# Kernel tuning notes

Hardware: AMD Instinct MI355X
Metric: run time of the kernel (lower is better)

## Reference

```python
import jax, jax.numpy as jnp
import numpy as np

WINDOW = 7
HEADS = 8


def setup_inputs() -> dict:
    key = jax.random.key(0)
    ks = jax.random.split(key, 6)
    B, L, C = 4096, WINDOW * WINDOW, 256
    x = jax.random.normal(ks[0], (B, L, C), dtype=jnp.float32)
    relative_index = jax.random.randint(ks[1], (L * L,), 0, (2 * WINDOW - 1) ** 2, dtype=jnp.int32)
    qkv_w = jax.random.normal(ks[2], (C, 3 * C), dtype=jnp.float32) * 0.02
    qkv_b = jnp.zeros((3 * C,), dtype=jnp.float32)
    rel_bias = jax.random.normal(ks[3], ((2 * WINDOW - 1) ** 2, HEADS), dtype=jnp.float32) * 0.02
    proj_w = jax.random.normal(ks[4], (C, C), dtype=jnp.float32) * 0.02
    proj_b = jnp.zeros((C,), dtype=jnp.float32)
    return {"x": x, "relative_index": relative_index, "qkv_w": qkv_w, "qkv_b": qkv_b,
            "rel_bias": rel_bias, "proj_w": proj_w, "proj_b": proj_b}


def reference(x, relative_index, qkv_w, qkv_b, rel_bias, proj_w, proj_b):
    B, L, C = x.shape
    H = HEADS
    D = C // H
    scale = D ** -0.5
    # qkv projection -> [3, B, H, L, D]
    qkv = (x @ qkv_w + qkv_b).reshape(B, L, 3, H, D).transpose(2, 0, 3, 1, 4)
    q, k, v = qkv[0], qkv[1], qkv[2]
    attn = jnp.einsum('bhld,bhmd->bhlm', q * scale, k)  # [B,H,L,L]
    # gather relative position bias: [L*L, H] -> [H, L, L]
    bias = rel_bias[relative_index].reshape(L, L, H).transpose(2, 0, 1)
    attn = jax.nn.softmax(attn + bias[None], axis=-1)
    out = jnp.einsum('bhlm,bhmd->blhd', attn, v).reshape(B, L, C)
    return out @ proj_w + proj_b
```

## Files before the change

### kernel.cpp

```cpp
#include <hip/hip_runtime.h>


typedef short s8v __attribute__((ext_vector_type(8)));
typedef short s4v __attribute__((ext_vector_type(4)));
typedef float f4  __attribute__((ext_vector_type(4)));

#define MFMA(a,b,c) __builtin_amdgcn_mfma_f32_16x16x32_bf16((a),(b),(c),0,0,0)

__device__ __forceinline__ unsigned short f2bf(float f) {
    unsigned u = __float_as_uint(f);
    u = u + 0x7fffu + ((u >> 16) & 1u);
    return (unsigned short)(u >> 16);
}

__device__ __forceinline__ unsigned pkbf(float lo, float hi) {
    unsigned r;
    asm("v_cvt_pk_bf16_f32 %0, %1, %2" : "=v"(r) : "v"(lo), "v"(hi));
    return r;
}

__global__ void prep(const float* __restrict__ qkv_w, const float* __restrict__ proj_w,
                     const float* __restrict__ rel_bias, const int* __restrict__ rel_idx,
                     unsigned short* __restrict__ wq, unsigned short* __restrict__ wp,
                     float* __restrict__ biasT2)
{
    int idx = blockIdx.x * blockDim.x + threadIdx.x;
    int stride = gridDim.x * blockDim.x;
    for (int i = idx; i < 48*8*64*8; i += stride) {
        int j = i & 7, l = (i >> 3) & 63, ks = (i >> 9) & 7, nt = i >> 12;
        int k = ks*32 + (l >> 4)*8 + j;
        int n = nt*16 + (l & 15);
        wq[i] = f2bf(qkv_w[k*768 + n]);
    }
    for (int i = idx; i < 16*8*64*8; i += stride) {
        int j = i & 7, l = (i >> 3) & 63, ks = (i >> 9) & 7, nt = i >> 12;
        int k = ks*32 + (l >> 4)*8 + j;
        int n = nt*16 + (l & 15);
        wp[i] = f2bf(proj_w[k*256 + n]);
    }
    for (int i = idx; i < 8*64*64; i += stride) {
        int k = i & 63, q = (i >> 6) & 63, h = i >> 12;
        float v;
        if (k < 49) v = (q < 49) ? rel_bias[rel_idx[q*49 + k]*8 + h] : 0.f;
        else        v = -1e30f;
        biasT2[i] = v;
    }
}

__global__ __launch_bounds__(512, 2) void kall(
    const float* __restrict__ x, const float* __restrict__ qkv_b,
    const unsigned short* __restrict__ wq, const float* __restrict__ biasT2,
    const unsigned short* __restrict__ wp, const float* __restrict__ proj_b,
    float* __restrict__ out)
{
    __shared__ __align__(16) unsigned short xs[4][8][64][8];
    __shared__ __align__(16) unsigned short osd[64][264];

    const int b    = blockIdx.x;
    const int tid  = threadIdx.x;
    const int w    = tid >> 6;
    const int lane = tid & 63;
    const int ln   = lane & 15;
    const int g    = lane >> 4;

    const float* xb = x + (size_t)b * (49*256);
    for (int i = tid; i < 4096; i += 512) {
        int r = i >> 6, c4 = i & 63;
        float4 v = make_float4(0.f, 0.f, 0.f, 0.f);
        if (r < 49) v = ((const float4*)xb)[r*64 + c4];
        uint2 o;
        o.x = pkbf(v.x, v.y);
        o.y = pkbf(v.z, v.w);
        int mt = r >> 4, lnr = r & 15;
        int c  = c4 * 4;
        int ks = c >> 5, gg = (c >> 3) & 3, j0 = c & 7;
        *(uint2*)&xs[mt][ks][(gg*16 + lnr) ^ ks][j0] = o;
    }
    __syncthreads();

    const float scale = 0.17677669529663687f;
    const int h = w;

    f4 qa[2][4], ka[2][4], va[4][2];
    #pragma unroll
    for (int dh = 0; dh < 2; ++dh)
        #pragma unroll
        for (int mt = 0; mt < 4; ++mt) {
            qa[dh][mt] = (f4){0.f,0.f,0.f,0.f};
            ka[dh][mt] = (f4){0.f,0.f,0.f,0.f};
            va[mt][dh] = (f4){0.f,0.f,0.f,0.f};
        }

    #pragma unroll
    for (int ks = 0; ks < 8; ++ks) {
        s8v xf[4];
        #pragma unroll
        for (int mt = 0; mt < 4; ++mt)
            xf[mt] = *(const s8v*)&xs[mt][ks][lane ^ ks][0];
        s8v wfq[2], wfk[2], wfv[2];
        #pragma unroll
        for (int dh = 0; dh < 2; ++dh) {
            wfq[dh] = *(const s8v*)&wq[(size_t)((( 2*h+dh)*8 + ks)*64 + lane) * 8];
            wfk[dh] = *(const s8v*)&wq[(size_t)(((16+2*h+dh)*8 + ks)*64 + lane) * 8];
            wfv[dh] = *(const s8v*)&wq[(size_t)(((32+2*h+dh)*8 + ks)*64 + lane) * 8];
        }
        #pragma unroll
        for (int dh = 0; dh < 2; ++dh)
            #pragma unroll
            for (int mt = 0; mt < 4; ++mt) {
                qa[dh][mt] = MFMA(wfq[dh], xf[mt], qa[dh][mt]);
                ka[dh][mt] = MFMA(wfk[dh], xf[mt], ka[dh][mt]);
                va[mt][dh] = MFMA(xf[mt], wfv[dh], va[mt][dh]);
            }
    }

    float4 bq[2], bk[2]; float bv[2];
    #pragma unroll
    for (int dh = 0; dh < 2; ++dh) {
        bq[dh] = *(const float4*)&qkv_b[       h*32 + dh*16 + g*4];
        bk[dh] = *(const float4*)&qkv_b[256 +  h*32 + dh*16 + g*4];
        bv[dh] = qkv_b[512 + h*32 + dh*16 + ln];
    }

    s8v qf[4], kf[4], vf[2][2];
    #pragma unroll
    for (int t = 0; t < 4; ++t) {
        union { s8v s; unsigned u[4]; } qu, ku;
        qu.u[0] = pkbf((qa[0][t][0] + bq[0].x)*scale, (qa[0][t][1] + bq[0].y)*scale);
        qu.u[1] = pkbf((qa[0][t][2] + bq[0].z)*scale, (qa[0][t][3] + bq[0].w)*scale);
        qu.u[2] = pkbf((qa[1][t][0] + bq[1].x)*scale, (qa[1][t][1] + bq[1].y)*scale);
        qu.u[3] = pkbf((qa[1][t][2] + bq[1].z)*scale, (qa[1][t][3] + bq[1].w)*scale);
        ku.u[0] = pkbf( ka[0][t][0] + bk[0].x,  ka[0][t][1] + bk[0].y);
        ku.u[1] = pkbf( ka[0][t][2] + bk[0].z,  ka[0][t][3] + bk[0].w);
        ku.u[2] = pkbf( ka[1][t][0] + bk[1].x,  ka[1][t][1] + bk[1].y);
        ku.u[3] = pkbf( ka[1][t][2] + bk[1].z,  ka[1][t][3] + bk[1].w);
        qf[t] = qu.s;
        kf[t] = ku.s;
    }
    #pragma unroll
    for (int ksp = 0; ksp < 2; ++ksp)
        #pragma unroll
        for (int dh = 0; dh < 2; ++dh) {
            union { s8v s; unsigned u[4]; } vu;
            vu.u[0] = pkbf(va[2*ksp  ][dh][0] + bv[dh], va[2*ksp  ][dh][1] + bv[dh]);
            vu.u[1] = pkbf(va[2*ksp  ][dh][2] + bv[dh], va[2*ksp  ][dh][3] + bv[dh]);
            vu.u[2] = pkbf(va[2*ksp+1][dh][0] + bv[dh], va[2*ksp+1][dh][1] + bv[dh]);
            vu.u[3] = pkbf(va[2*ksp+1][dh][2] + bv[dh], va[2*ksp+1][dh][3] + bv[dh]);
            vf[ksp][dh] = vu.s;
        }

    #pragma unroll
    for (int qt = 0; qt < 4; ++qt) {
        f4 bias4[4];
        #pragma unroll
        for (int kt = 0; kt < 4; ++kt)
            bias4[kt] = *(const f4*)&biasT2[(size_t)(h*64 + qt*16 + ln)*64 + kt*16 + g*4];

        __builtin_amdgcn_s_setprio(1);
        f4 st[4];
        #pragma unroll
        for (int kt = 0; kt < 4; ++kt) {
            f4 z = (f4){0.f,0.f,0.f,0.f};
            st[kt] = MFMA(kf[kt], qf[qt], z);
        }
        __builtin_amdgcn_s_setprio(0);

        float pr[16];
        float sum = 0.f;
        #pragma unroll
        for (int kt = 0; kt < 4; ++kt)
            #pragma unroll
            for (int r = 0; r < 4; ++r) {
                float e = __expf(st[kt][r] + bias4[kt][r]);
                pr[kt*4 + r] = e;
                sum += e;
            }
        sum += __shfl_xor(sum, 16);
        sum += __shfl_xor(sum, 32);
        float rinv = 1.f / sum;

        s8v pa[2];
        #pragma unroll
        for (int ksp = 0; ksp < 2; ++ksp) {
            union { s8v s; unsigned u[4]; } pu;
            #pragma unroll
            for (int i2 = 0; i2 < 4; ++i2)
                pu.u[i2] = pkbf(pr[8*ksp + 2*i2] * rinv, pr[8*ksp + 2*i2 + 1] * rinv);
            pa[ksp] = pu.s;
        }

        __builtin_amdgcn_s_setprio(1);
        f4 oacc[2];
        oacc[0] = (f4){0.f,0.f,0.f,0.f};
        oacc[1] = (f4){0.f,0.f,0.f,0.f};
        #pragma unroll
        for (int ksp = 0; ksp < 2; ++ksp)
            #pragma unroll
            for (int dh = 0; dh < 2; ++dh)
                oacc[dh] = MFMA(pa[ksp], vf[ksp][dh], oacc[dh]);
        __builtin_amdgcn_s_setprio(0);

        #pragma unroll
        for (int dh = 0; dh < 2; ++dh)
            #pragma unroll
            for (int r = 0; r < 4; ++r)
                osd[qt*16 + g*4 + r][h*32 + dh*16 + ln] = f2bf(oacc[dh][r]);
    }
    __syncthreads();

    f4 acc[4][2];
    #pragma unroll
    for (int mt = 0; mt < 4; ++mt)
        #pragma unroll
        for (int t = 0; t < 2; ++t)
            acc[mt][t] = (f4){0.f,0.f,0.f,0.f};

    #pragma unroll
    for (int ks = 0; ks < 8; ++ks) {
        s8v av[4], bw[2];
        #pragma unroll
        for (int mt = 0; mt < 4; ++mt)
            av[mt] = *(const s8v*)&osd[mt*16 + ln][ks*32 + g*8];
        #pragma unroll
        for (int t = 0; t < 2; ++t) {
            int nt = w*2 + t;
            bw[t] = *(const s8v*)&wp[(size_t)((nt*8 + ks)*64 + lane) * 8];
        }
        #pragma unroll
        for (int mt = 0; mt < 4; ++mt)
            #pragma unroll
            for (int t = 0; t < 2; ++t)
                acc[mt][t] = MFMA(av[mt], bw[t], acc[mt][t]);
    }

    float* ob = out + (size_t)b * (49*256);
    #pragma unroll
    for (int t = 0; t < 2; ++t) {
        int n = (w*2 + t)*16 + ln;
        float pb = proj_b[n];
        #pragma unroll
        for (int mt = 0; mt < 4; ++mt)
            #pragma unroll
            for (int r = 0; r < 4; ++r) {
                int q = mt*16 + g*4 + r;
                if (q < 49)
                    ob[q*256 + n] = acc[mt][t][r] + pb;
            }
    }
}

extern "C" void kernel_launch(void* const* d_in, const int* in_sizes, int n_in,
                              void* d_out, int out_size, void* d_ws, size_t ws_size,
                              hipStream_t stream)
{
    (void)n_in; (void)out_size; (void)ws_size;
    const float* x        = (const float*)d_in[0];
    const int*   rel_idx  = (const int*)  d_in[1];
    const float* qkv_w    = (const float*)d_in[2];
    const float* qkv_b    = (const float*)d_in[3];
    const float* rel_bias = (const float*)d_in[4];
    const float* proj_w   = (const float*)d_in[5];
    const float* proj_b   = (const float*)d_in[6];
    float* out = (float*)d_out;

    const int B = in_sizes[0] / (49*256);

    unsigned short* wq = (unsigned short*)d_ws;
    unsigned short* wp = wq + 48*8*64*8;
    float* biasT2 = (float*)((char*)d_ws + 524288);

    prep<<<256, 256, 0, stream>>>(qkv_w, proj_w, rel_bias, rel_idx, wq, wp, biasT2);
    kall<<<B, 512, 0, stream>>>(x, qkv_b, wq, biasT2, wp, proj_b, out);
}
```

Measured before the change: 274.0 us.

## Process eight windows per block with double-buffered register prefetch of x

Each block now loops over 8 windows instead of one. The next window's x is loaded into registers during the QKV MFMA phase and written into a second LDS buffer before attention, so global load latency overlaps with compute. This amortizes block launch and bias setup, but the grid shrinks to 512 blocks. That leaves fewer blocks than CUs times occupancy, and register pressure rises from the 8 float4 prefetch registers.

```diff
diff --git a/kernel.cpp b/kernel.cpp
--- a/kernel.cpp
+++ b/kernel.cpp
@@ -2,7 +2,6 @@
 
 
 typedef short s8v __attribute__((ext_vector_type(8)));
-typedef short s4v __attribute__((ext_vector_type(4)));
 typedef float f4  __attribute__((ext_vector_type(4)));
 
 #define MFMA(a,b,c) __builtin_amdgcn_mfma_f32_16x16x32_bf16((a),(b),(c),0,0,0)
@@ -17,6 +16,34 @@
     unsigned r;
     asm("v_cvt_pk_bf16_f32 %0, %1, %2" : "=v"(r) : "v"(lo), "v"(hi));
     return r;
+}
+
+__device__ __forceinline__ void load_pf(const float* __restrict__ xb,
+                                        float4 pf[8], int tid) {
+    #pragma unroll
+    for (int ii = 0; ii < 8; ++ii) {
+        int i = tid + ii*512;
+        float4 v = make_float4(0.f, 0.f, 0.f, 0.f);
+        if ((i >> 6) < 49) v = ((const float4*)xb)[i];
+        pf[ii] = v;
+    }
+}
+
+__device__ __forceinline__ void cvt_write_xs(const float4 pf[8],
+                                             unsigned short (*xsb)[8][64][8],
+                                             int tid) {
+    #pragma unroll
+    for (int ii = 0; ii < 8; ++ii) {
+        int i = tid + ii*512;
+        int r = i >> 6, c4 = i & 63;
+        uint2 o;
+        o.x = pkbf(pf[ii].x, pf[ii].y);
+        o.y = pkbf(pf[ii].z, pf[ii].w);
+        int mt = r >> 4, lnr = r & 15;
+        int c  = c4 * 4;
+        int ks = c >> 5, gg = (c >> 3) & 3, j0 = c & 7;
+        *(uint2*)&xsb[mt][ks][(gg*16 + lnr) ^ ks][j0] = o;
+    }
 }
 
 __global__ void prep(const float* __restrict__ qkv_w, const float* __restrict__ proj_w,
@@ -51,68 +78,23 @@
     const float* __restrict__ x, const float* __restrict__ qkv_b,
     const unsigned short* __restrict__ wq, const float* __restrict__ biasT2,
     const unsigned short* __restrict__ wp, const float* __restrict__ proj_b,
-    float* __restrict__ out)
+    float* __restrict__ out, int B)
 {
-    __shared__ __align__(16) unsigned short xs[4][8][64][8];
+    __shared__ __align__(16) unsigned short xs2[2][4][8][64][8];
     __shared__ __align__(16) unsigned short osd[64][264];
 
-    const int b    = blockIdx.x;
     const int tid  = threadIdx.x;
     const int w    = tid >> 6;
     const int lane = tid & 63;
     const int ln   = lane & 15;
     const int g    = lane >> 4;
 
-    const float* xb = x + (size_t)b * (49*256);
-    for (int i = tid; i < 4096; i += 512) {
-        int r = i >> 6, c4 = i & 63;
-        float4 v = make_float4(0.f, 0.f, 0.f, 0.f);
-        if (r < 49) v = ((const float4*)xb)[r*64 + c4];
-        uint2 o;
-        o.x = pkbf(v.x, v.y);
-        o.y = pkbf(v.z, v.w);
-        int mt = r >> 4, lnr = r & 15;
-        int c  = c4 * 4;
-        int ks = c >> 5, gg = (c >> 3) & 3, j0 = c & 7;
-        *(uint2*)&xs[mt][ks][(gg*16 + lnr) ^ ks][j0] = o;
-    }
-    __syncthreads();
+    const int W    = 8;
+    const int win0 = blockIdx.x * W;
+    const int nw   = (B - win0 < W) ? (B - win0) : W;
 
     const float scale = 0.17677669529663687f;
     const int h = w;
-
-    f4 qa[2][4], ka[2][4], va[4][2];
-    #pragma unroll
-    for (int dh = 0; dh < 2; ++dh)
-        #pragma unroll
-        for (int mt = 0; mt < 4; ++mt) {
-            qa[dh][mt] = (f4){0.f,0.f,0.f,0.f};
-            ka[dh][mt] = (f4){0.f,0.f,0.f,0.f};
-            va[mt][dh] = (f4){0.f,0.f,0.f,0.f};
-        }
-
-    #pragma unroll
-    for (int ks = 0; ks < 8; ++ks) {
-        s8v xf[4];
-        #pragma unroll
-        for (int mt = 0; mt < 4; ++mt)
-            xf[mt] = *(const s8v*)&xs[mt][ks][lane ^ ks][0];
-        s8v wfq[2], wfk[2], wfv[2];
-        #pragma unroll
-        for (int dh = 0; dh < 2; ++dh) {
-            wfq[dh] = *(const s8v*)&wq[(size_t)((( 2*h+dh)*8 + ks)*64 + lane) * 8];
-            wfk[dh] = *(const s8v*)&wq[(size_t)(((16+2*h+dh)*8 + ks)*64 + lane) * 8];
-            wfv[dh] = *(const s8v*)&wq[(size_t)(((32+2*h+dh)*8 + ks)*64 + lane) * 8];
-        }
-        #pragma unroll
-        for (int dh = 0; dh < 2; ++dh)
-            #pragma unroll
-            for (int mt = 0; mt < 4; ++mt) {
-                qa[dh][mt] = MFMA(wfq[dh], xf[mt], qa[dh][mt]);
-                ka[dh][mt] = MFMA(wfk[dh], xf[mt], ka[dh][mt]);
-                va[mt][dh] = MFMA(xf[mt], wfv[dh], va[mt][dh]);
-            }
-    }
 
     float4 bq[2], bk[2]; float bv[2];
     #pragma unroll
@@ -122,130 +104,179 @@
         bv[dh] = qkv_b[512 + h*32 + dh*16 + ln];
     }
 
-    s8v qf[4], kf[4], vf[2][2];
-    #pragma unroll
-    for (int t = 0; t < 4; ++t) {
-        union { s8v s; unsigned u[4]; } qu, ku;
-        qu.u[0] = pkbf((qa[0][t][0] + bq[0].x)*scale, (qa[0][t][1] + bq[0].y)*scale);
-        qu.u[1] = pkbf((qa[0][t][2] + bq[0].z)*scale, (qa[0][t][3] + bq[0].w)*scale);
-        qu.u[2] = pkbf((qa[1][t][0] + bq[1].x)*scale, (qa[1][t][1] + bq[1].y)*scale);
-        qu.u[3] = pkbf((qa[1][t][2] + bq[1].z)*scale, (qa[1][t][3] + bq[1].w)*scale);
-        ku.u[0] = pkbf( ka[0][t][0] + bk[0].x,  ka[0][t][1] + bk[0].y);
-        ku.u[1] = pkbf( ka[0][t][2] + bk[0].z,  ka[0][t][3] + bk[0].w);
-        ku.u[2] = pkbf( ka[1][t][0] + bk[1].x,  ka[1][t][1] + bk[1].y);
-        ku.u[3] = pkbf( ka[1][t][2] + bk[1].z,  ka[1][t][3] + bk[1].w);
-        qf[t] = qu.s;
-        kf[t] = ku.s;
-    }
-    #pragma unroll
-    for (int ksp = 0; ksp < 2; ++ksp)
-        #pragma unroll
-        for (int dh = 0; dh < 2; ++dh) {
-            union { s8v s; unsigned u[4]; } vu;
-            vu.u[0] = pkbf(va[2*ksp  ][dh][0] + bv[dh], va[2*ksp  ][dh][1] + bv[dh]);
-            vu.u[1] = pkbf(va[2*ksp  ][dh][2] + bv[dh], va[2*ksp  ][dh][3] + bv[dh]);
-            vu.u[2] = pkbf(va[2*ksp+1][dh][0] + bv[dh], va[2*ksp+1][dh][1] + bv[dh]);
-            vu.u[3] = pkbf(va[2*ksp+1][dh][2] + bv[dh], va[2*ksp+1][dh][3] + bv[dh]);
-            vf[ksp][dh] = vu.s;
-        }
-
-    #pragma unroll
-    for (int qt = 0; qt < 4; ++qt) {
-        f4 bias4[4];
-        #pragma unroll
-        for (int kt = 0; kt < 4; ++kt)
-            bias4[kt] = *(const f4*)&biasT2[(size_t)(h*64 + qt*16 + ln)*64 + kt*16 + g*4];
-
-        __builtin_amdgcn_s_setprio(1);
-        f4 st[4];
-        #pragma unroll
-        for (int kt = 0; kt < 4; ++kt) {
-            f4 z = (f4){0.f,0.f,0.f,0.f};
-            st[kt] = MFMA(kf[kt], qf[qt], z);
-        }
-        __builtin_amdgcn_s_setprio(0);
-
-        float pr[16];
-        float sum = 0.f;
-        #pragma unroll
-        for (int kt = 0; kt < 4; ++kt)
-            #pragma unroll
-            for (int r = 0; r < 4; ++r) {
-                float e = __expf(st[kt][r] + bias4[kt][r]);
-                pr[kt*4 + r] = e;
-                sum += e;
-            }
-        sum += __shfl_xor(sum, 16);
-        sum += __shfl_xor(sum, 32);
-        float rinv = 1.f / sum;
-
-        s8v pa[2];
-        #pragma unroll
-        for (int ksp = 0; ksp < 2; ++ksp) {
-            union { s8v s; unsigned u[4]; } pu;
-            #pragma unroll
-            for (int i2 = 0; i2 < 4; ++i2)
-                pu.u[i2] = pkbf(pr[8*ksp + 2*i2] * rinv, pr[8*ksp + 2*i2 + 1] * rinv);
-            pa[ksp] = pu.s;
-        }
-
-        __builtin_amdgcn_s_setprio(1);
-        f4 oacc[2];
-        oacc[0] = (f4){0.f,0.f,0.f,0.f};
-        oacc[1] = (f4){0.f,0.f,0.f,0.f};
+    float4 pf[8];
+    load_pf(x + (size_t)win0 * (49*256), pf, tid);
+    cvt_write_xs(pf, xs2[0], tid);
+    __syncthreads();
+
+    for (int iw = 0; iw < nw; ++iw) {
+        const int b = win0 + iw;
+        unsigned short (*xsb)[8][64][8] = xs2[iw & 1];
+        const bool hn = (iw + 1 < nw);
+
+        if (hn) load_pf(x + (size_t)(b+1) * (49*256), pf, tid);
+
+        f4 qa[2][4], ka[2][4], va[4][2];
+        #pragma unroll
+        for (int dh = 0; dh < 2; ++dh)
+            #pragma unroll
+            for (int mt = 0; mt < 4; ++mt) {
+                qa[dh][mt] = (f4){0.f,0.f,0.f,0.f};
+                ka[dh][mt] = (f4){0.f,0.f,0.f,0.f};
+                va[mt][dh] = (f4){0.f,0.f,0.f,0.f};
+            }
+
+        #pragma unroll
+        for (int ks = 0; ks < 8; ++ks) {
+            s8v xf[4];
+            #pragma unroll
+            for (int mt = 0; mt < 4; ++mt)
+                xf[mt] = *(const s8v*)&xsb[mt][ks][lane ^ ks][0];
+            s8v wfq[2], wfk[2], wfv[2];
+            #pragma unroll
+            for (int dh = 0; dh < 2; ++dh) {
+                wfq[dh] = *(const s8v*)&wq[(size_t)((( 2*h+dh)*8 + ks)*64 + lane) * 8];
+                wfk[dh] = *(const s8v*)&wq[(size_t)(((16+2*h+dh)*8 + ks)*64 + lane) * 8];
+                wfv[dh] = *(const s8v*)&wq[(size_t)(((32+2*h+dh)*8 + ks)*64 + lane) * 8];
+            }
+            #pragma unroll
+            for (int dh = 0; dh < 2; ++dh)
+                #pragma unroll
+                for (int mt = 0; mt < 4; ++mt) {
+                    qa[dh][mt] = MFMA(wfq[dh], xf[mt], qa[dh][mt]);
+                    ka[dh][mt] = MFMA(wfk[dh], xf[mt], ka[dh][mt]);
+                    va[mt][dh] = MFMA(xf[mt], wfv[dh], va[mt][dh]);
+                }
+        }
+
+        s8v qf[4], kf[4], vf[2][2];
+        #pragma unroll
+        for (int t = 0; t < 4; ++t) {
+            union { s8v s; unsigned u[4]; } qu, ku;
+            qu.u[0] = pkbf((qa[0][t][0] + bq[0].x)*scale, (qa[0][t][1] + bq[0].y)*scale);
+            qu.u[1] = pkbf((qa[0][t][2] + bq[0].z)*scale, (qa[0][t][3] + bq[0].w)*scale);
+            qu.u[2] = pkbf((qa[1][t][0] + bq[1].x)*scale, (qa[1][t][1] + bq[1].y)*scale);
+            qu.u[3] = pkbf((qa[1][t][2] + bq[1].z)*scale, (qa[1][t][3] + bq[1].w)*scale);
+            ku.u[0] = pkbf( ka[0][t][0] + bk[0].x,  ka[0][t][1] + bk[0].y);
+            ku.u[1] = pkbf( ka[0][t][2] + bk[0].z,  ka[0][t][3] + bk[0].w);
+            ku.u[2] = pkbf( ka[1][t][0] + bk[1].x,  ka[1][t][1] + bk[1].y);
+            ku.u[3] = pkbf( ka[1][t][2] + bk[1].z,  ka[1][t][3] + bk[1].w);
+            qf[t] = qu.s;
+            kf[t] = ku.s;
+        }
         #pragma unroll
         for (int ksp = 0; ksp < 2; ++ksp)
             #pragma unroll
+            for (int dh = 0; dh < 2; ++dh) {
+                union { s8v s; unsigned u[4]; } vu;
+                vu.u[0] = pkbf(va[2*ksp  ][dh][0] + bv[dh], va[2*ksp  ][dh][1] + bv[dh]);
+                vu.u[1] = pkbf(va[2*ksp  ][dh][2] + bv[dh], va[2*ksp  ][dh][3] + bv[dh]);
+                vu.u[2] = pkbf(va[2*ksp+1][dh][0] + bv[dh], va[2*ksp+1][dh][1] + bv[dh]);
+                vu.u[3] = pkbf(va[2*ksp+1][dh][2] + bv[dh], va[2*ksp+1][dh][3] + bv[dh]);
+                vf[ksp][dh] = vu.s;
+            }
+
+        if (hn) cvt_write_xs(pf, xs2[(iw + 1) & 1], tid);
+
+        #pragma unroll
+        for (int qt = 0; qt < 4; ++qt) {
+            f4 bias4[4];
+            #pragma unroll
+            for (int kt = 0; kt < 4; ++kt)
+                bias4[kt] = *(const f4*)&biasT2[(size_t)(h*64 + qt*16 + ln)*64 + kt*16 + g*4];
+
+            __builtin_amdgcn_s_setprio(1);
+            f4 st[4];
+            #pragma unroll
+            for (int kt = 0; kt < 4; ++kt) {
+                f4 z = (f4){0.f,0.f,0.f,0.f};
+                st[kt] = MFMA(kf[kt], qf[qt], z);
+            }
+            __builtin_amdgcn_s_setprio(0);
+
+            float pr[16];
+            float sum = 0.f;
+            #pragma unroll
+            for (int kt = 0; kt < 4; ++kt)
+                #pragma unroll
+                for (int r = 0; r < 4; ++r) {
+                    float e = __expf(st[kt][r] + bias4[kt][r]);
+                    pr[kt*4 + r] = e;
+                    sum += e;
+                }
+            sum += __shfl_xor(sum, 16);
+            sum += __shfl_xor(sum, 32);
+            float rinv = 1.f / sum;
+
+            s8v pa[2];
+            #pragma unroll
+            for (int ksp = 0; ksp < 2; ++ksp) {
+                union { s8v s; unsigned u[4]; } pu;
+                #pragma unroll
+                for (int i2 = 0; i2 < 4; ++i2)
+                    pu.u[i2] = pkbf(pr[8*ksp + 2*i2] * rinv, pr[8*ksp + 2*i2 + 1] * rinv);
+                pa[ksp] = pu.s;
+            }
+
+            __builtin_amdgcn_s_setprio(1);
+            f4 oacc[2];
+            oacc[0] = (f4){0.f,0.f,0.f,0.f};
+            oacc[1] = (f4){0.f,0.f,0.f,0.f};
+            #pragma unroll
+            for (int ksp = 0; ksp < 2; ++ksp)
+                #pragma unroll
+                for (int dh = 0; dh < 2; ++dh)
+                    oacc[dh] = MFMA(pa[ksp], vf[ksp][dh], oacc[dh]);
+            __builtin_amdgcn_s_setprio(0);
+
+            #pragma unroll
             for (int dh = 0; dh < 2; ++dh)
-                oacc[dh] = MFMA(pa[ksp], vf[ksp][dh], oacc[dh]);
-        __builtin_amdgcn_s_setprio(0);
-
-        #pragma unroll
-        for (int dh = 0; dh < 2; ++dh)
-            #pragma unroll
-            for (int r = 0; r < 4; ++r)
-                osd[qt*16 + g*4 + r][h*32 + dh*16 + ln] = f2bf(oacc[dh][r]);
-    }
-    __syncthreads();
-
-    f4 acc[4][2];
-    #pragma unroll
-    for (int mt = 0; mt < 4; ++mt)
-        #pragma unroll
-        for (int t = 0; t < 2; ++t)
-            acc[mt][t] = (f4){0.f,0.f,0.f,0.f};
-
-    #pragma unroll
-    for (int ks = 0; ks < 8; ++ks) {
-        s8v av[4], bw[2];
+                #pragma unroll
+                for (int r = 0; r < 4; ++r)
+                    osd[qt*16 + g*4 + r][h*32 + dh*16 + ln] = f2bf(oacc[dh][r]);
+        }
+        __syncthreads();
+
+        f4 acc[4][2];
         #pragma unroll
         for (int mt = 0; mt < 4; ++mt)
-            av[mt] = *(const s8v*)&osd[mt*16 + ln][ks*32 + g*8];
+            #pragma unroll
+            for (int t = 0; t < 2; ++t)
+                acc[mt][t] = (f4){0.f,0.f,0.f,0.f};
+
+        #pragma unroll
+        for (int ks = 0; ks < 8; ++ks) {
+            s8v av[4], bw[2];
+            #pragma unroll
+            for (int mt = 0; mt < 4; ++mt)
+                av[mt] = *(const s8v*)&osd[mt*16 + ln][ks*32 + g*8];
+            #pragma unroll
+            for (int t = 0; t < 2; ++t) {
+                int nt = w*2 + t;
+                bw[t] = *(const s8v*)&wp[(size_t)((nt*8 + ks)*64 + lane) * 8];
+            }
+            #pragma unroll
+            for (int mt = 0; mt < 4; ++mt)
+                #pragma unroll
+                for (int t = 0; t < 2; ++t)
+                    acc[mt][t] = MFMA(av[mt], bw[t], acc[mt][t]);
+        }
+
+        float* ob = out + (size_t)b * (49*256);
         #pragma unroll
         for (int t = 0; t < 2; ++t) {
-            int nt = w*2 + t;
-            bw[t] = *(const s8v*)&wp[(size_t)((nt*8 + ks)*64 + lane) * 8];
-        }
-        #pragma unroll
-        for (int mt = 0; mt < 4; ++mt)
-            #pragma unroll
-            for (int t = 0; t < 2; ++t)
-                acc[mt][t] = MFMA(av[mt], bw[t], acc[mt][t]);
-    }
-
-    float* ob = out + (size_t)b * (49*256);
-    #pragma unroll
-    for (int t = 0; t < 2; ++t) {
-        int n = (w*2 + t)*16 + ln;
-        float pb = proj_b[n];
-        #pragma unroll
-        for (int mt = 0; mt < 4; ++mt)
-            #pragma unroll
-            for (int r = 0; r < 4; ++r) {
-                int q = mt*16 + g*4 + r;
-                if (q < 49)
-                    ob[q*256 + n] = acc[mt][t][r] + pb;
-            }
+            int n = (w*2 + t)*16 + ln;
+            float pb = proj_b[n];
+            #pragma unroll
+            for (int mt = 0; mt < 4; ++mt)
+                #pragma unroll
+                for (int r = 0; r < 4; ++r) {
+                    int q = mt*16 + g*4 + r;
+                    if (q < 49)
+                        ob[q*256 + n] = acc[mt][t][r] + pb;
+                }
+        }
+        __syncthreads();
     }
 }
 
@@ -264,11 +295,13 @@
     float* out = (float*)d_out;
 
     const int B = in_sizes[0] / (49*256);
+    const int W = 8;
+    const int nb = (B + W - 1) / W;
 
     unsigned short* wq = (unsigned short*)d_ws;
     unsigned short* wp = wq + 48*8*64*8;
     float* biasT2 = (float*)((char*)d_ws + 524288);
 
     prep<<<256, 256, 0, stream>>>(qkv_w, proj_w, rel_bias, rel_idx, wq, wp, biasT2);
-    kall<<<B, 512, 0, stream>>>(x, qkv_b, wq, biasT2, wp, proj_b, out);
-}
+    kall<<<nb, 512, 0, stream>>>(x, qkv_b, wq, biasT2, wp, proj_b, out, B);
+}
```

Result: slower. 704.3 us (+157.1%).
